# Kernel tuning notes

Measured on AMD Instinct MI355X. Metric: run time of the kernel, lower is better.

Reference implementation:

```python
import jax, jax.numpy as jnp
import numpy as np

N_NODES = 100000
N_EDGES = 3200000
D = 32


def _gat(x, edge_index, W, att_s, att_d, bias, heads, ch, neg_slope):
    """PyG-style GATConv (shared lin for src/dst, add_self_loops=False).
    x: [N, D_in], edge_index: [2, E], W: [heads*ch, D_in],
    att_s/att_d: [heads, ch], bias: [heads*ch]. Returns [N, heads*ch]."""
    n = x.shape[0]
    h = (x @ W.T).reshape(n, heads, ch)                      # [N,H,C]
    a_s = (h * att_s[None]).sum(-1)                           # [N,H]
    a_d = (h * att_d[None]).sum(-1)                           # [N,H]
    src, dst = edge_index[0], edge_index[1]
    logits = jax.nn.leaky_relu(a_s[src] + a_d[dst], neg_slope)  # [E,H]
    # segment softmax over edges grouped by destination node
    m = jax.ops.segment_max(logits, dst, num_segments=n)     # [N,H]
    m = jnp.where(jnp.isfinite(m), m, 0.0)                    # nodes w/ no in-edges
    ex = jnp.exp(logits - m[dst])                             # [E,H]
    denom = jax.ops.segment_sum(ex, dst, num_segments=n)     # [N,H]
    alpha = ex / (denom[dst] + 1e-16)                         # [E,H]
    out = jax.ops.segment_sum(alpha[:, :, None] * h[src], dst, num_segments=n)  # [N,H,C]
    return out.reshape(n, heads * ch) + bias


def setup_inputs() -> dict:
    key = jax.random.key(0)
    ks = jax.random.split(key, 16)
    x = jax.random.normal(ks[0], (N_NODES, D), dtype=jnp.float32)
    edge_index = jax.random.randint(ks[1], (2, N_EDGES), 0, N_NODES, dtype=jnp.int64)
    s = 1.0 / np.sqrt(D)
    return {
        "x": x,
        "edge_index": edge_index,
        "W1": jax.random.normal(ks[2], (32, D), dtype=jnp.float32) * s,
        "att_s1": jax.random.normal(ks[3], (2, 16), dtype=jnp.float32) * 0.05,
        "att_d1": jax.random.normal(ks[4], (2, 16), dtype=jnp.float32) * 0.05,
        "b1": jnp.full((32,), 0.1, dtype=jnp.float32),
        "ea1": jnp.ones((1,), dtype=jnp.float32),  # edge_activator
        "W2": jax.random.normal(ks[5], (32, 32), dtype=jnp.float32) * s,
        "att_s2": jax.random.normal(ks[6], (2, 16), dtype=jnp.float32) * 0.05,
        "att_d2": jax.random.normal(ks[7], (2, 16), dtype=jnp.float32) * 0.05,
        "b2": jnp.full((32,), 0.1, dtype=jnp.float32),
        "W3": jax.random.normal(ks[8], (32, 32), dtype=jnp.float32) * s,
        "att_s3": jax.random.normal(ks[9], (1, 32), dtype=jnp.float32) * 0.05,
        "att_d3": jax.random.normal(ks[10], (1, 32), dtype=jnp.float32) * 0.05,
        "b3": jnp.full((32,), 0.1, dtype=jnp.float32),
    }


def reference(x, edge_index, W1, att_s1, att_d1, b1, ea1,
              W2, att_s2, att_d2, b2, W3, att_s3, att_d3, b3):
    # --- layer 1 (negative_slope=0.01) ---
    h = _gat(x, edge_index, W1, att_s1, att_d1, b1, heads=2, ch=16, neg_slope=0.01)
    scale = jnp.tanh(ea1)[0]
    scale = jnp.where(scale < 0.1, 1.0, scale)  # 'continue' branch skips the scaling
    h = h * scale
    h = h + 0.05 * jax.lax.stop_gradient(h)      # h + 0.05*h.detach()
    h = jax.nn.elu(h)                            # eval path (training=False)
    h = jnp.clip(h, -3.0, 3.0)
    # --- layer 2 (default negative_slope=0.2) ---
    h = _gat(h, edge_index, W2, att_s2, att_d2, b2, heads=2, ch=16, neg_slope=0.2)
    h = jax.nn.elu(h)
    h = jnp.clip(h, -3.0, 3.0)
    # --- layer 3: heads=1, concat=False ---
    out = _gat(h, edge_index, W3, att_s3, att_d3, b3, heads=1, ch=32, neg_slope=0.2)
    return out
```

## Files before the change

### kernel.cpp

```cpp
#include <hip/hip_runtime.h>
#include <hip/hip_bf16.h>
#include <hip/hip_fp16.h>


#define NPB  128
#define CAPB 6144
#define PAD_SENTINEL 0xFFFFFFFFu

template <int H, int NL>
__device__ __forceinline__ void transform_body(
    const float* __restrict__ in, const float* __restrict__ W,
    const float* __restrict__ att_s, const float* __restrict__ att_d,
    __half* __restrict__ h16, float* __restrict__ a_s, float* __restrict__ a_d,
    int node0, int nlim, float (*Wl)[33], float (*xs)[32]) {
    constexpr int C = 32 / H;
    constexpr int NTH = NL * 32;
    int t = threadIdx.x;
    for (int i = t; i < 1024; i += NTH) Wl[i >> 5][i & 31] = W[i];
    int nl = t >> 5, o = t & 31;
    int node = node0 + nl;
    xs[nl][o] = (node < nlim) ? in[(size_t)node * 32 + o] : 0.f;
    __syncthreads();
    float acc = 0.f;
#pragma unroll
    for (int k = 0; k < 32; k++) acc = fmaf(xs[nl][k], Wl[o][k], acc);
    if (node < nlim) {
        h16[(size_t)node * 32 + o] = __float2half_rn(acc);
        float vs = acc * att_s[o];
        float vd = acc * att_d[o];
#pragma unroll
        for (int m = C / 2; m >= 1; m >>= 1) {
            vs += __shfl_xor(vs, m, 64);
            vd += __shfl_xor(vd, m, 64);
        }
        if ((o % C) == 0) {
            int hh = o / C;
            a_s[node * H + hh] = vs;
            a_d[node * H + hh] = vd;
        }
    }
}

__global__ void __launch_bounds__(1024)
k_bin_t1(const int* __restrict__ src, const int* __restrict__ dst,
         int* __restrict__ bucket_cursor, unsigned int* __restrict__ pairs,
         int e, int nb, int nbb,
         const float* __restrict__ in, const float* __restrict__ W,
         const float* __restrict__ att_s, const float* __restrict__ att_d,
         __half* __restrict__ h16, float* __restrict__ a_s,
         float* __restrict__ a_d, int nsplit) {
    __shared__ union {
        struct { int h[1024]; int bs[1024]; int cb[1024]; unsigned int stage[8192]; } b;
        struct { float Wl[32][33]; float xs[32][32]; } t;
    } sh;
    int t = threadIdx.x;
    if ((int)blockIdx.x >= nbb) {
        int node0 = ((int)blockIdx.x - nbb) * 32;
        transform_body<2, 32>(in, W, att_s, att_d, h16, a_s, a_d,
                              node0, nsplit, sh.t.Wl, sh.t.xs);
        return;
    }
    sh.b.h[t] = 0;
    __syncthreads();
    int e4 = e >> 2;
    int base4 = blockIdx.x * 2048;
    int boff[8];
    unsigned int pk[8];
#pragma unroll
    for (int k = 0; k < 2; k++) {
        int i4 = base4 + k * 1024 + t;
        if (i4 < e4) {
            int4 dv = ((const int4*)dst)[i4];
            int4 sv = ((const int4*)src)[i4];
            const int* dd = (const int*)&dv;
            const int* ss = (const int*)&sv;
#pragma unroll
            for (int j = 0; j < 4; j++) {
                int q = 4 * k + j;
                int d = dd[j];
                int b = d >> 7;
                pk[q] = ((unsigned int)ss[j] << 7) | (unsigned int)(d & 127);
                int off = atomicAdd(&sh.b.h[b], 1);
                boff[q] = (b << 16) | off;
            }
        } else {
#pragma unroll
            for (int j = 0; j < 4; j++) boff[4 * k + j] = -1;
        }
    }
    __syncthreads();
    if (t >= 128 && t - 128 < nb) {
        int b = t - 128;
        int c = sh.b.h[b];
        sh.b.cb[b] = c ? atomicAdd(&bucket_cursor[b], c) : 0;
    }
    if (t < 64) {
        int sum = 0;
#pragma unroll
        for (int j = 0; j < 16; j++) sum += sh.b.h[t * 16 + j];
        int run = sum;
#pragma unroll
        for (int off = 1; off < 64; off <<= 1) {
            int v = __shfl_up(run, off, 64);
            if (t >= off) run += v;
        }
        int base = run - sum;
#pragma unroll
        for (int j = 0; j < 16; j++) {
            int b = t * 16 + j;
            sh.b.bs[b] = base;
            base += sh.b.h[b];
        }
    }
    __syncthreads();
#pragma unroll
    for (int q = 0; q < 8; q++) {
        if (boff[q] >= 0) {
            int b = boff[q] >> 16;
            sh.b.stage[sh.b.bs[b] + (boff[q] & 0xFFFF)] = pk[q];
        }
    }
    __syncthreads();
    int wv = t >> 6, ln = t & 63;
    for (int b = wv; b < nb; b += 16) {
        int c = sh.b.h[b];
        if (c == 0) continue;
        int gb = sh.b.cb[b];
        int room = CAPB - gb;
        if (c > room) c = (room > 0) ? room : 0;
        unsigned int* dp = pairs + (size_t)b * CAPB + gb;
        const unsigned int* sp = sh.b.stage + sh.b.bs[b];
        for (int o = ln; o < c; o += 64) dp[o] = sp[o];
    }
    if (blockIdx.x == 0 && t < (e & 3)) {
        int i = (e & ~3) + t;
        int d = dst[i];
        int b = d >> 7;
        int r = atomicAdd(&bucket_cursor[b], 1);
        if (r < CAPB)
            pairs[(size_t)b * CAPB + r] =
                ((unsigned int)src[i] << 7) | (unsigned int)(d & 127);
    }
}

__global__ void __launch_bounds__(512)
k_sort_t1(const unsigned int* __restrict__ pairs,
          const int* __restrict__ bucket_cursor,
          int2* __restrict__ rowinfo, int* __restrict__ src_sorted,
          int n, int nb,
          const float* __restrict__ in, const float* __restrict__ W,
          const float* __restrict__ att_s, const float* __restrict__ att_d,
          __half* __restrict__ h16, float* __restrict__ a_s,
          float* __restrict__ a_d, int nsplit) {
    __shared__ union {
        struct { int cnt[NPB]; int cur[NPB]; int total;
                 unsigned int lp[CAPB]; int op[CAPB]; } s;
        struct { float Wl[32][33]; float xs[16][32]; } t;
    } sh;
    int t = threadIdx.x;
    if ((int)blockIdx.x >= nb) {
        int node0 = nsplit + ((int)blockIdx.x - nb) * 16;
        transform_body<2, 16>(in, W, att_s, att_d, h16, a_s, a_d,
                              node0, n, sh.t.Wl, sh.t.xs);
        return;
    }
    int b = blockIdx.x;
    int bbase = b * CAPB;
    int m = bucket_cursor[b];
    if (m > CAPB) m = CAPB;
    if (t < NPB) sh.s.cnt[t] = 0;
    __syncthreads();
    for (int cb = 0; cb < m; cb += 4096) {
        unsigned int pv[8];
#pragma unroll
        for (int u = 0; u < 8; u++) {
            int i = cb + u * 512 + t;
            pv[u] = (i < m) ? pairs[bbase + i] : PAD_SENTINEL;
        }
#pragma unroll
        for (int u = 0; u < 8; u++) {
            int i = cb + u * 512 + t;
            if (i < m) sh.s.lp[i] = pv[u];
            if (pv[u] != PAD_SENTINEL) atomicAdd(&sh.s.cnt[pv[u] & 127], 1);
        }
    }
    __syncthreads();
    if (t < 64) {
        int c0 = sh.s.cnt[2 * t];
        int c1 = sh.s.cnt[2 * t + 1];
        int sum = c0 + c1;
        int run = sum;
#pragma unroll
        for (int off = 1; off < 64; off <<= 1) {
            int v = __shfl_up(run, off, 64);
            if (t >= off) run += v;
        }
        int ex = run - sum;
        sh.s.cur[2 * t] = ex;
        sh.s.cur[2 * t + 1] = ex + c0;
        int node = b * NPB + 2 * t;
        if (node < n) rowinfo[node] = make_int2(bbase + ex, c0);
        if (node + 1 < n) rowinfo[node + 1] = make_int2(bbase + ex + c0, c1);
        if (t == 63) sh.s.total = run;
    }
    __syncthreads();
    for (int cb = 0; cb < m; cb += 4096) {
        unsigned int pv[8];
        int of[8];
#pragma unroll
        for (int u = 0; u < 8; u++) {
            int i = cb + u * 512 + t;
            pv[u] = (i < m) ? sh.s.lp[i] : PAD_SENTINEL;
        }
#pragma unroll
        for (int u = 0; u < 8; u++)
            if (pv[u] != PAD_SENTINEL) of[u] = atomicAdd(&sh.s.cur[pv[u] & 127], 1);
#pragma unroll
        for (int u = 0; u < 8; u++)
            if (pv[u] != PAD_SENTINEL) sh.s.op[of[u]] = (int)(pv[u] >> 7);
    }
    __syncthreads();
    int nt4 = (sh.s.total + 3) >> 2;
    int4* dst4 = (int4*)(src_sorted + bbase);
    const int4* src4 = (const int4*)sh.s.op;
    for (int i = t; i < nt4; i += 512) dst4[i] = src4[i];
}

#define PB_LOAD(Qa, Qb, Qc, Qd, H0, H1, H2_, H3_, H4_, H5_, H6_, H7_, B)      \
    Qa = *(const int4*)(lb + (B) * 2);                                        \
    Qb = *(const int4*)(lb + (B) * 2 + 8);                                    \
    Qc = *(const int4*)(lb + (B) * 2 + 16);                                   \
    Qd = *(const int4*)(lb + (B) * 2 + 24);                                   \
    H0 = *(const __half2*)(hbase + (unsigned)((Qa.x << 6) + co));             \
    H1 = *(const __half2*)(hbase + (unsigned)((Qa.z << 6) + co));             \
    H2_ = *(const __half2*)(hbase + (unsigned)((Qb.x << 6) + co));            \
    H3_ = *(const __half2*)(hbase + (unsigned)((Qb.z << 6) + co));            \
    H4_ = *(const __half2*)(hbase + (unsigned)((Qc.x << 6) + co));            \
    H5_ = *(const __half2*)(hbase + (unsigned)((Qc.z << 6) + co));            \
    H6_ = *(const __half2*)(hbase + (unsigned)((Qd.x << 6) + co));            \
    H7_ = *(const __half2*)(hbase + (unsigned)((Qd.z << 6) + co));

#define PB_FMA(Qa, Qb, Qc, Qd, H0, H1, H2_, H3_, H4_, H5_, H6_, H7_)          \
    {                                                                         \
        float xa0 = __int_as_float(Qa.y), xa1 = __int_as_float(Qa.w);         \
        float xb0 = __int_as_float(Qb.y), xb1 = __int_as_float(Qb.w);         \
        float xc0 = __int_as_float(Qc.y), xc1 = __int_as_float(Qc.w);         \
        float xd0 = __int_as_float(Qd.y), xd1 = __int_as_float(Qd.w);         \
        acc0 = fmaf(xa0, __half2float(__low2half(H0)), acc0);                 \
        acc1 = fmaf(xa0, __half2float(__high2half(H0)), acc1);                \
        acc0 = fmaf(xa1, __half2float(__low2half(H1)), acc0);                 \
        acc1 = fmaf(xa1, __half2float(__high2half(H1)), acc1);                \
        acc0 = fmaf(xb0, __half2float(__low2half(H2_)), acc0);                \
        acc1 = fmaf(xb0, __half2float(__high2half(H2_)), acc1);               \
        acc0 = fmaf(xb1, __half2float(__low2half(H3_)), acc0);                \
        acc1 = fmaf(xb1, __half2float(__high2half(H3_)), acc1);               \
        acc0 = fmaf(xc0, __half2float(__low2half(H4_)), acc0);                \
        acc1 = fmaf(xc0, __half2float(__high2half(H4_)), acc1);               \
        acc0 = fmaf(xc1, __half2float(__low2half(H5_)), acc0);                \
        acc1 = fmaf(xc1, __half2float(__high2half(H5_)), acc1);               \
        acc0 = fmaf(xd0, __half2float(__low2half(H6_)), acc0);                \
        acc1 = fmaf(xd0, __half2float(__high2half(H6_)), acc1);               \
        acc0 = fmaf(xd1, __half2float(__low2half(H7_)), acc0);                \
        acc1 = fmaf(xd1, __half2float(__high2half(H7_)), acc1);               \
    }

#define PB_PIPELINED_LOOP                                                     \
    {                                                                         \
        int4 qa, qb, qc, qd, na, nb2, nc, nd;                                 \
        __half2 h0, h1, h2, h3, h4, h5, h6, h7;                               \
        __half2 g0, g1, g2, g3, g4, g5, g6, g7;                               \
        PB_LOAD(qa, qb, qc, qd, h0, h1, h2, h3, h4, h5, h6, h7, 0)            \
        for (int base = 0; base < padB; base += 16) {                         \
            int nxt = base + 16;                                              \
            if (nxt < padB) {                                                 \
                PB_LOAD(na, nb2, nc, nd, g0, g1, g2, g3, g4, g5, g6, g7, nxt) \
            }                                                                 \
            PB_FMA(qa, qb, qc, qd, h0, h1, h2, h3, h4, h5, h6, h7)            \
            qa = na; qb = nb2; qc = nc; qd = nd;                              \
            h0 = g0; h1 = g1; h2 = g2; h3 = g3;                               \
            h4 = g4; h5 = g5; h6 = g6; h7 = g7;                               \
        }                                                                     \
    }

template <int H, int EPI, int H2>
__global__ void __launch_bounds__(256)
k_edge_f(const int2* __restrict__ rowinfo, const int* __restrict__ src_sorted,
         const __half* __restrict__ h16,
         const float* __restrict__ a_s, const float* __restrict__ a_d,
         const float* __restrict__ bias, const float* __restrict__ ea,
         const float* __restrict__ Wn, const float* __restrict__ att_sn,
         const float* __restrict__ att_dn,
         __half* __restrict__ h16n, float* __restrict__ a_sn,
         float* __restrict__ a_dn, int n, float slope) {
    constexpr int CAP = 96;
    constexpr int RSTR = 2 * CAP + 16;
    __shared__ int lds_raw[8][H][RSTR];
    __shared__ float Wl2[32][33];
    __shared__ float row[8][32];
    int t = threadIdx.x;
    for (int i = t; i < 1024; i += 256) Wl2[i >> 5][i & 31] = Wn[i];
    __syncthreads();
    int nw = t >> 5;
    int hl = t & 31;
    int node = blockIdx.x * 8 + nw;
    if (node >= n) return;
    float ats = att_sn[hl], atd = att_dn[hl];
    int2 bi = rowinfo[node];
    int beg = bi.x, deg = bi.y;
    int padB = (deg + 15) & ~15;

    float ad[H];
#pragma unroll
    for (int hh = 0; hh < H; hh++) ad[hh] = a_d[node * H + hh];

    float ds[H];
#pragma unroll
    for (int hh = 0; hh < H; hh++) ds[hh] = 0.f;
    bool fast = (padB <= CAP);
    if (fast) {
        for (int idx = hl; idx < padB; idx += 32) {
            if (idx < deg) {
                int s = src_sorted[beg + idx];
                if (H == 2) {
                    float2 as2 = *(const float2*)((const char*)a_s + (unsigned)(s << 3));
                    float l0 = as2.x + ad[0]; l0 = fmaxf(l0, l0 * slope);
                    float l1 = as2.y + ad[1]; l1 = fmaxf(l1, l1 * slope);
                    float e0 = __expf(l0), e1 = __expf(l1);
                    ds[0] += e0; ds[1] += e1;
                    ((int2*)lds_raw[nw][0])[idx] = make_int2(s, __float_as_int(e0));
                    ((int2*)lds_raw[nw][H - 1])[idx] = make_int2(s, __float_as_int(e1));
                } else {
                    float l0 = a_s[s] + ad[0]; l0 = fmaxf(l0, l0 * slope);
                    float e0 = __expf(l0);
                    ds[0] += e0;
                    ((int2*)lds_raw[nw][0])[idx] = make_int2(s, __float_as_int(e0));
                }
            } else {
#pragma unroll
                for (int hh = 0; hh < H; hh++)
                    ((int2*)lds_raw[nw][hh])[idx] = make_int2(0, 0);
            }
        }
    } else {
        for (int idx = hl; idx < deg; idx += 32) {
            int s = src_sorted[beg + idx];
            if (H == 2) {
                float2 as2 = *(const float2*)((const char*)a_s + (unsigned)(s << 3));
                float l0 = as2.x + ad[0]; l0 = fmaxf(l0, l0 * slope);
                float l1 = as2.y + ad[1]; l1 = fmaxf(l1, l1 * slope);
                ds[0] += __expf(l0); ds[1] += __expf(l1);
            } else {
                float l0 = a_s[s] + ad[0]; l0 = fmaxf(l0, l0 * slope);
                ds[0] += __expf(l0);
            }
        }
    }

    int e2 = hl >> 4;
    int l16 = hl & 15;
    int hd = (H == 2) ? (l16 >> 3) : 0;
    int co = l16 << 2;
    float adh = ad[hd];
    float acc0 = 0.f, acc1 = 0.f;
    const char* hbase = (const char*)h16;
    const int* lb = &lds_raw[nw][hd][e2 * 4];

    if (fast) {
        PB_PIPELINED_LOOP
    } else {
        for (int base = 0; base < deg; base += 16) {
#pragma unroll
            for (int u = 0; u < 8; u++) {
                int idx = base + u * 2 + e2;
                int s = 0;
                float ex = 0.f;
                if (idx < deg) {
                    s = src_sorted[beg + idx];
                    float l = a_s[s * H + hd] + adh;
                    l = fmaxf(l, l * slope);
                    ex = __expf(l);
                }
                __half2 hv = *(const __half2*)(hbase + (unsigned)((s << 6) + co));
                acc0 = fmaf(ex, __half2float(__low2half(hv)), acc0);
                acc1 = fmaf(ex, __half2float(__high2half(hv)), acc1);
            }
        }
    }

#pragma unroll
    for (int hh = 0; hh < H; hh++) {
        float v = ds[hh];
#pragma unroll
        for (int m = 16; m >= 1; m >>= 1) v += __shfl_xor(v, m, 64);
        ds[hh] = 1.f / (v + 1e-16f);
    }
    acc0 += __shfl_xor(acc0, 16, 64);
    acc1 += __shfl_xor(acc1, 16, 64);

    float invd = ds[hd];
    float2 bv = *(const float2*)(bias + l16 * 2);
    float v0 = fmaf(acc0, invd, bv.x);
    float v1 = fmaf(acc1, invd, bv.y);
    if (EPI == 1) {
        float s0 = tanhf(ea[0]);
        if (s0 < 0.1f) s0 = 1.0f;
        s0 *= 1.05f;
        v0 *= s0; v1 *= s0;
    }
    v0 = (v0 > 0.f) ? v0 : expm1f(v0);
    v1 = (v1 > 0.f) ? v1 : expm1f(v1);
    v0 = fminf(3.f, fmaxf(-3.f, v0));
    v1 = fminf(3.f, fmaxf(-3.f, v1));

    if (hl < 16) {
        row[nw][2 * l16] = v0;
        row[nw][2 * l16 + 1] = v1;
    }
    float acc = 0.f;
#pragma unroll
    for (int k = 0; k < 32; k++) acc = fmaf(row[nw][k], Wl2[hl][k], acc);
    h16n[(size_t)node * 32 + hl] = __float2half_rn(acc);
    float vs = acc * ats;
    float vd = acc * atd;
    constexpr int C2 = 32 / H2;
#pragma unroll
    for (int m = C2 / 2; m >= 1; m >>= 1) {
        vs += __shfl_xor(vs, m, 64);
        vd += __shfl_xor(vd, m, 64);
    }
    if ((hl % C2) == 0) {
        int hh = hl / C2;
        a_sn[node * H2 + hh] = vs;
        a_dn[node * H2 + hh] = vd;
    }
}

template <int H, int EPI>
__global__ void k_edge(const int2* __restrict__ rowinfo, const int* __restrict__ src_sorted,
                       const __half* __restrict__ h16,
                       const float* __restrict__ a_s, const float* __restrict__ a_d,
                       const float* __restrict__ bias, const float* __restrict__ ea,
                       float* __restrict__ out, int n, float slope) {
    constexpr int CAP = 96;
    constexpr int RSTR = 2 * CAP + 16;
    __shared__ int lds_raw[8][H][RSTR];
    int nw = threadIdx.x >> 5;
    int hl = threadIdx.x & 31;
    int node = blockIdx.x * 8 + nw;
    if (node >= n) return;
    int2 bi = rowinfo[node];
    int beg = bi.x, deg = bi.y;
    int padB = (deg + 15) & ~15;

    float ad[H];
#pragma unroll
    for (int hh = 0; hh < H; hh++) ad[hh] = a_d[node * H + hh];

    float ds[H];
#pragma unroll
    for (int hh = 0; hh < H; hh++) ds[hh] = 0.f;
    bool fast = (padB <= CAP);
    if (fast) {
        for (int idx = hl; idx < padB; idx += 32) {
            if (idx < deg) {
                int s = src_sorted[beg + idx];
                if (H == 2) {
                    float2 as2 = *(const float2*)((const char*)a_s + (unsigned)(s << 3));
                    float l0 = as2.x + ad[0]; l0 = fmaxf(l0, l0 * slope);
                    float l1 = as2.y + ad[1]; l1 = fmaxf(l1, l1 * slope);
                    float e0 = __expf(l0), e1 = __expf(l1);
                    ds[0] += e0; ds[1] += e1;
                    ((int2*)lds_raw[nw][0])[idx] = make_int2(s, __float_as_int(e0));
                    ((int2*)lds_raw[nw][H - 1])[idx] = make_int2(s, __float_as_int(e1));
                } else {
                    float l0 = a_s[s] + ad[0]; l0 = fmaxf(l0, l0 * slope);
                    float e0 = __expf(l0);
                    ds[0] += e0;
                    ((int2*)lds_raw[nw][0])[idx] = make_int2(s, __float_as_int(e0));
                }
            } else {
#pragma unroll
                for (int hh = 0; hh < H; hh++)
                    ((int2*)lds_raw[nw][hh])[idx] = make_int2(0, 0);
            }
        }
    } else {
        for (int idx = hl; idx < deg; idx += 32) {
            int s = src_sorted[beg + idx];
            if (H == 2) {
                float2 as2 = *(const float2*)((const char*)a_s + (unsigned)(s << 3));
                float l0 = as2.x + ad[0]; l0 = fmaxf(l0, l0 * slope);
                float l1 = as2.y + ad[1]; l1 = fmaxf(l1, l1 * slope);
                ds[0] += __expf(l0); ds[1] += __expf(l1);
            } else {
                float l0 = a_s[s] + ad[0]; l0 = fmaxf(l0, l0 * slope);
                ds[0] += __expf(l0);
            }
        }
    }

    int e2 = hl >> 4;
    int l16 = hl & 15;
    int hd = (H == 2) ? (l16 >> 3) : 0;
    int co = l16 << 2;
    float adh = ad[hd];
    float acc0 = 0.f, acc1 = 0.f;
    const char* hbase = (const char*)h16;
    const int* lb = &lds_raw[nw][hd][e2 * 4];

    if (fast) {
        PB_PIPELINED_LOOP
    } else {
        for (int base = 0; base < deg; base += 16) {
#pragma unroll
            for (int u = 0; u < 8; u++) {
                int idx = base + u * 2 + e2;
                int s = 0;
                float ex = 0.f;
                if (idx < deg) {
                    s = src_sorted[beg + idx];
                    float l = a_s[s * H + hd] + adh;
                    l = fmaxf(l, l * slope);
                    ex = __expf(l);
                }
                __half2 hv = *(const __half2*)(hbase + (unsigned)((s << 6) + co));
                acc0 = fmaf(ex, __half2float(__low2half(hv)), acc0);
                acc1 = fmaf(ex, __half2float(__high2half(hv)), acc1);
            }
        }
    }

#pragma unroll
    for (int hh = 0; hh < H; hh++) {
        float v = ds[hh];
#pragma unroll
        for (int m = 16; m >= 1; m >>= 1) v += __shfl_xor(v, m, 64);
        ds[hh] = 1.f / (v + 1e-16f);
    }
    acc0 += __shfl_xor(acc0, 16, 64);
    acc1 += __shfl_xor(acc1, 16, 64);

    if (l16 == hl) {
        float invd = ds[hd];
        float2 bv = *(const float2*)(bias + l16 * 2);
        float v0 = fmaf(acc0, invd, bv.x);
        float v1 = fmaf(acc1, invd, bv.y);
        if (EPI == 1) {
            float s0 = tanhf(ea[0]);
            if (s0 < 0.1f) s0 = 1.0f;
            s0 *= 1.05f;
            v0 *= s0; v1 *= s0;
            v0 = (v0 > 0.f) ? v0 : expm1f(v0);
            v1 = (v1 > 0.f) ? v1 : expm1f(v1);
            v0 = fminf(3.f, fmaxf(-3.f, v0));
            v1 = fminf(3.f, fmaxf(-3.f, v1));
        } else if (EPI == 2) {
            v0 = (v0 > 0.f) ? v0 : expm1f(v0);
            v1 = (v1 > 0.f) ? v1 : expm1f(v1);
            v0 = fminf(3.f, fmaxf(-3.f, v0));
            v1 = fminf(3.f, fmaxf(-3.f, v1));
        }
        *(float2*)(out + (size_t)node * 32 + l16 * 2) = make_float2(v0, v1);
    }
}

extern "C" void kernel_launch(void* const* d_in, const int* in_sizes, int n_in,
                              void* d_out, int out_size, void* d_ws, size_t ws_size,
                              hipStream_t stream) {
    const float* x   = (const float*)d_in[0];
    const int*   ei  = (const int*)d_in[1];
    const float* W1  = (const float*)d_in[2];
    const float* as1 = (const float*)d_in[3];
    const float* ad1 = (const float*)d_in[4];
    const float* b1  = (const float*)d_in[5];
    const float* ea1 = (const float*)d_in[6];
    const float* W2  = (const float*)d_in[7];
    const float* as2 = (const float*)d_in[8];
    const float* ad2 = (const float*)d_in[9];
    const float* b2  = (const float*)d_in[10];
    const float* W3  = (const float*)d_in[11];
    const float* as3 = (const float*)d_in[12];
    const float* ad3 = (const float*)d_in[13];
    const float* b3  = (const float*)d_in[14];
    float* out = (float*)d_out;

    const int n = in_sizes[0] / 32;
    const int e = in_sizes[1] / 2;
    const int* src = ei;
    const int* dst = ei + e;
    const int nb = (n + NPB - 1) / NPB;

    char* w = (char*)d_ws;
    auto alloc = [&](size_t bytes) -> void* {
        void* p = (void*)w;
        w += (bytes + 255) & ~(size_t)255;
        return p;
    };
    __half* h16a    = (__half*)alloc((size_t)n * 32 * 2);
    float* a_s1     = (float*)alloc((size_t)n * 2 * 4);
    float* a_d1     = (float*)alloc((size_t)n * 2 * 4);
    int2* rowinfo   = (int2*)alloc((size_t)n * 8);
    int* bucket_cur = (int*)alloc((size_t)(nb + 1) * 4);
    int* src_sorted = (int*)alloc((size_t)nb * CAPB * 4);
    unsigned int* pairs = (unsigned int*)alloc((size_t)nb * CAPB * 4);

    char* sc = (char*)pairs;
    auto carve = [&](size_t bytes) -> void* {
        void* p = (void*)sc;
        sc += (bytes + 255) & ~(size_t)255;
        return p;
    };
    __half* h16b = (__half*)carve((size_t)n * 32 * 2);
    float* a_s2  = (float*)carve((size_t)n * 2 * 4);
    float* a_d2  = (float*)carve((size_t)n * 2 * 4);
    float* a_s3  = (float*)carve((size_t)n * 4);
    float* a_d3  = (float*)carve((size_t)n * 4);

    int nsplit = n / 2;
    nsplit = (nsplit + 31) & ~31;
    if (nsplit > n) nsplit = n;
    const int t1a = (nsplit + 31) / 32;
    const int t1b = (n - nsplit + 15) / 16;
    int e4 = e >> 2;
    const int nbb = (e4 + 2047) / 2048;

    hipMemsetAsync(bucket_cur, 0, (size_t)nb * 4, stream);
    k_bin_t1<<<nbb + t1a, 1024, 0, stream>>>(src, dst, bucket_cur, pairs, e, nb, nbb,
                                             x, W1, as1, ad1, h16a, a_s1, a_d1, nsplit);
    k_sort_t1<<<nb + t1b, 512, 0, stream>>>(pairs, bucket_cur, rowinfo, src_sorted, n, nb,
                                            x, W1, as1, ad1, h16a, a_s1, a_d1, nsplit);

    const int egrid = (n + 7) / 8;

    k_edge_f<2, 1, 2><<<egrid, 256, 0, stream>>>(rowinfo, src_sorted, h16a, a_s1, a_d1,
                                                 b1, ea1, W2, as2, ad2,
                                                 h16b, a_s2, a_d2, n, 0.01f);
    k_edge_f<2, 2, 1><<<egrid, 256, 0, stream>>>(rowinfo, src_sorted, h16b, a_s2, a_d2,
                                                 b2, nullptr, W3, as3, ad3,
                                                 h16a, a_s3, a_d3, n, 0.2f);
    k_edge<1, 0><<<egrid, 256, 0, stream>>>(rowinfo, src_sorted, h16a, a_s3, a_d3,
                                            b3, nullptr, out, n, 0.2f);
}
```

Before: 307.5 us.

## Gather full 16-byte feature chunks per lane with 8 edges per pass

Changes the edge aggregation lane mapping in both edge kernels. Each group of 4 lanes now covers one edge and each lane loads an int4 (8 halves) of the source row, so 8 edges are processed per pass instead of each lane loading a 4-byte half2 across 16-edge pipelined blocks. The intent is fewer, wider gather instructions per edge. In exchange it drops the explicit software prefetch pipeline, adds a 3-step 8-register shuffle reduction, and runs the epilogue with 8 values per lane using float4 stores.

```diff
diff --git a/kernel.cpp b/kernel.cpp
--- a/kernel.cpp
+++ b/kernel.cpp
@@ -226,60 +226,20 @@
     for (int i = t; i < nt4; i += 512) dst4[i] = src4[i];
 }
 
-#define PB_LOAD(Qa, Qb, Qc, Qd, H0, H1, H2_, H3_, H4_, H5_, H6_, H7_, B)      \
-    Qa = *(const int4*)(lb + (B) * 2);                                        \
-    Qb = *(const int4*)(lb + (B) * 2 + 8);                                    \
-    Qc = *(const int4*)(lb + (B) * 2 + 16);                                   \
-    Qd = *(const int4*)(lb + (B) * 2 + 24);                                   \
-    H0 = *(const __half2*)(hbase + (unsigned)((Qa.x << 6) + co));             \
-    H1 = *(const __half2*)(hbase + (unsigned)((Qa.z << 6) + co));             \
-    H2_ = *(const __half2*)(hbase + (unsigned)((Qb.x << 6) + co));            \
-    H3_ = *(const __half2*)(hbase + (unsigned)((Qb.z << 6) + co));            \
-    H4_ = *(const __half2*)(hbase + (unsigned)((Qc.x << 6) + co));            \
-    H5_ = *(const __half2*)(hbase + (unsigned)((Qc.z << 6) + co));            \
-    H6_ = *(const __half2*)(hbase + (unsigned)((Qd.x << 6) + co));            \
-    H7_ = *(const __half2*)(hbase + (unsigned)((Qd.z << 6) + co));
-
-#define PB_FMA(Qa, Qb, Qc, Qd, H0, H1, H2_, H3_, H4_, H5_, H6_, H7_)          \
+#define PB25_FMA(HV)                                                          \
     {                                                                         \
-        float xa0 = __int_as_float(Qa.y), xa1 = __int_as_float(Qa.w);         \
-        float xb0 = __int_as_float(Qb.y), xb1 = __int_as_float(Qb.w);         \
-        float xc0 = __int_as_float(Qc.y), xc1 = __int_as_float(Qc.w);         \
-        float xd0 = __int_as_float(Qd.y), xd1 = __int_as_float(Qd.w);         \
-        acc0 = fmaf(xa0, __half2float(__low2half(H0)), acc0);                 \
-        acc1 = fmaf(xa0, __half2float(__high2half(H0)), acc1);                \
-        acc0 = fmaf(xa1, __half2float(__low2half(H1)), acc0);                 \
-        acc1 = fmaf(xa1, __half2float(__high2half(H1)), acc1);                \
-        acc0 = fmaf(xb0, __half2float(__low2half(H2_)), acc0);                \
-        acc1 = fmaf(xb0, __half2float(__high2half(H2_)), acc1);               \
-        acc0 = fmaf(xb1, __half2float(__low2half(H3_)), acc0);                \
-        acc1 = fmaf(xb1, __half2float(__high2half(H3_)), acc1);               \
-        acc0 = fmaf(xc0, __half2float(__low2half(H4_)), acc0);                \
-        acc1 = fmaf(xc0, __half2float(__high2half(H4_)), acc1);               \
-        acc0 = fmaf(xc1, __half2float(__low2half(H5_)), acc0);                \
-        acc1 = fmaf(xc1, __half2float(__high2half(H5_)), acc1);               \
-        acc0 = fmaf(xd0, __half2float(__low2half(H6_)), acc0);                \
-        acc1 = fmaf(xd0, __half2float(__high2half(H6_)), acc1);               \
-        acc0 = fmaf(xd1, __half2float(__low2half(H7_)), acc0);                \
-        acc1 = fmaf(xd1, __half2float(__high2half(H7_)), acc1);               \
-    }
-
-#define PB_PIPELINED_LOOP                                                     \
-    {                                                                         \
-        int4 qa, qb, qc, qd, na, nb2, nc, nd;                                 \
-        __half2 h0, h1, h2, h3, h4, h5, h6, h7;                               \
-        __half2 g0, g1, g2, g3, g4, g5, g6, g7;                               \
-        PB_LOAD(qa, qb, qc, qd, h0, h1, h2, h3, h4, h5, h6, h7, 0)            \
-        for (int base = 0; base < padB; base += 16) {                         \
-            int nxt = base + 16;                                              \
-            if (nxt < padB) {                                                 \
-                PB_LOAD(na, nb2, nc, nd, g0, g1, g2, g3, g4, g5, g6, g7, nxt) \
-            }                                                                 \
-            PB_FMA(qa, qb, qc, qd, h0, h1, h2, h3, h4, h5, h6, h7)            \
-            qa = na; qb = nb2; qc = nc; qd = nd;                              \
-            h0 = g0; h1 = g1; h2 = g2; h3 = g3;                               \
-            h4 = g4; h5 = g5; h6 = g6; h7 = g7;                               \
-        }                                                                     \
+        __half2 p0 = *(__half2*)&HV.x;                                        \
+        __half2 p1 = *(__half2*)&HV.y;                                        \
+        __half2 p2 = *(__half2*)&HV.z;                                        \
+        __half2 p3 = *(__half2*)&HV.w;                                        \
+        av[0] = fmaf(ex, __half2float(__low2half(p0)), av[0]);                \
+        av[1] = fmaf(ex, __half2float(__high2half(p0)), av[1]);               \
+        av[2] = fmaf(ex, __half2float(__low2half(p1)), av[2]);                \
+        av[3] = fmaf(ex, __half2float(__high2half(p1)), av[3]);               \
+        av[4] = fmaf(ex, __half2float(__low2half(p2)), av[4]);                \
+        av[5] = fmaf(ex, __half2float(__high2half(p2)), av[5]);               \
+        av[6] = fmaf(ex, __half2float(__low2half(p3)), av[6]);                \
+        av[7] = fmaf(ex, __half2float(__high2half(p3)), av[7]);               \
     }
 
 template <int H, int EPI, int H2>
@@ -356,35 +316,43 @@
         }
     }
 
-    int e2 = hl >> 4;
-    int l16 = hl & 15;
-    int hd = (H == 2) ? (l16 >> 3) : 0;
-    int co = l16 << 2;
-    float adh = ad[hd];
-    float acc0 = 0.f, acc1 = 0.f;
+    int q4 = hl & 3;
+    int eo = hl >> 2;
+    int hd2 = (H == 2) ? (q4 >> 1) : 0;
+    float adh = ad[hd2];
+    float av[8];
+#pragma unroll
+    for (int k = 0; k < 8; k++) av[k] = 0.f;
     const char* hbase = (const char*)h16;
-    const int* lb = &lds_raw[nw][hd][e2 * 4];
+    const int2* stp = (const int2*)&lds_raw[nw][hd2][0];
 
     if (fast) {
-        PB_PIPELINED_LOOP
+        for (int base = 0; base < padB; base += 8) {
+            int2 se = stp[base + eo];
+            float ex = __int_as_float(se.y);
+            int4 hv = *(const int4*)(hbase + (unsigned)((se.x << 6) + (q4 << 4)));
+            PB25_FMA(hv)
+        }
     } else {
-        for (int base = 0; base < deg; base += 16) {
-#pragma unroll
-            for (int u = 0; u < 8; u++) {
-                int idx = base + u * 2 + e2;
-                int s = 0;
-                float ex = 0.f;
-                if (idx < deg) {
-                    s = src_sorted[beg + idx];
-                    float l = a_s[s * H + hd] + adh;
-                    l = fmaxf(l, l * slope);
-                    ex = __expf(l);
-                }
-                __half2 hv = *(const __half2*)(hbase + (unsigned)((s << 6) + co));
-                acc0 = fmaf(ex, __half2float(__low2half(hv)), acc0);
-                acc1 = fmaf(ex, __half2float(__high2half(hv)), acc1);
-            }
-        }
+        for (int base = 0; base < deg; base += 8) {
+            int idx = base + eo;
+            int s = 0;
+            float ex = 0.f;
+            if (idx < deg) {
+                s = src_sorted[beg + idx];
+                float l = a_s[s * H + hd2] + adh;
+                l = fmaxf(l, l * slope);
+                ex = __expf(l);
+            }
+            int4 hv = *(const int4*)(hbase + (unsigned)((s << 6) + (q4 << 4)));
+            PB25_FMA(hv)
+        }
+    }
+
+#pragma unroll
+    for (int m = 4; m <= 16; m <<= 1) {
+#pragma unroll
+        for (int k = 0; k < 8; k++) av[k] += __shfl_xor(av[k], m, 64);
     }
 
 #pragma unroll
@@ -394,28 +362,37 @@
         for (int m = 16; m >= 1; m >>= 1) v += __shfl_xor(v, m, 64);
         ds[hh] = 1.f / (v + 1e-16f);
     }
-    acc0 += __shfl_xor(acc0, 16, 64);
-    acc1 += __shfl_xor(acc1, 16, 64);
-
-    float invd = ds[hd];
-    float2 bv = *(const float2*)(bias + l16 * 2);
-    float v0 = fmaf(acc0, invd, bv.x);
-    float v1 = fmaf(acc1, invd, bv.y);
+    float invd = ds[hd2];
+
+    float4 bv0 = *(const float4*)(bias + q4 * 8);
+    float4 bv1 = *(const float4*)(bias + q4 * 8 + 4);
+    float v[8];
+    v[0] = fmaf(av[0], invd, bv0.x);
+    v[1] = fmaf(av[1], invd, bv0.y);
+    v[2] = fmaf(av[2], invd, bv0.z);
+    v[3] = fmaf(av[3], invd, bv0.w);
+    v[4] = fmaf(av[4], invd, bv1.x);
+    v[5] = fmaf(av[5], invd, bv1.y);
+    v[6] = fmaf(av[6], invd, bv1.z);
+    v[7] = fmaf(av[7], invd, bv1.w);
     if (EPI == 1) {
         float s0 = tanhf(ea[0]);
         if (s0 < 0.1f) s0 = 1.0f;
         s0 *= 1.05f;
-        v0 *= s0; v1 *= s0;
-    }
-    v0 = (v0 > 0.f) ? v0 : expm1f(v0);
-    v1 = (v1 > 0.f) ? v1 : expm1f(v1);
-    v0 = fminf(3.f, fmaxf(-3.f, v0));
-    v1 = fminf(3.f, fmaxf(-3.f, v1));
-
-    if (hl < 16) {
-        row[nw][2 * l16] = v0;
-        row[nw][2 * l16 + 1] = v1;
-    }
+#pragma unroll
+        for (int k = 0; k < 8; k++) v[k] *= s0;
+    }
+#pragma unroll
+    for (int k = 0; k < 8; k++) {
+        v[k] = (v[k] > 0.f) ? v[k] : expm1f(v[k]);
+        v[k] = fminf(3.f, fmaxf(-3.f, v[k]));
+    }
+
+    if (eo == 0) {
+        *(float4*)&row[nw][q4 * 8]     = make_float4(v[0], v[1], v[2], v[3]);
+        *(float4*)&row[nw][q4 * 8 + 4] = make_float4(v[4], v[5], v[6], v[7]);
+    }
+
     float acc = 0.f;
 #pragma unroll
     for (int k = 0; k < 32; k++) acc = fmaf(row[nw][k], Wl2[hl][k], acc);
@@ -499,35 +476,43 @@
         }
     }
 
-    int e2 = hl >> 4;
-    int l16 = hl & 15;
-    int hd = (H == 2) ? (l16 >> 3) : 0;
-    int co = l16 << 2;
-    float adh = ad[hd];
-    float acc0 = 0.f, acc1 = 0.f;
+    int q4 = hl & 3;
+    int eo = hl >> 2;
+    int hd2 = (H == 2) ? (q4 >> 1) : 0;
+    float adh = ad[hd2];
+    float av[8];
+#pragma unroll
+    for (int k = 0; k < 8; k++) av[k] = 0.f;
     const char* hbase = (const char*)h16;
-    const int* lb = &lds_raw[nw][hd][e2 * 4];
+    const int2* stp = (const int2*)&lds_raw[nw][hd2][0];
 
     if (fast) {
-        PB_PIPELINED_LOOP
+        for (int base = 0; base < padB; base += 8) {
+            int2 se = stp[base + eo];
+            float ex = __int_as_float(se.y);
+            int4 hv = *(const int4*)(hbase + (unsigned)((se.x << 6) + (q4 << 4)));
+            PB25_FMA(hv)
+        }
     } else {
-        for (int base = 0; base < deg; base += 16) {
-#pragma unroll
-            for (int u = 0; u < 8; u++) {
-                int idx = base + u * 2 + e2;
-                int s = 0;
-                float ex = 0.f;
-                if (idx < deg) {
-                    s = src_sorted[beg + idx];
-                    float l = a_s[s * H + hd] + adh;
-                    l = fmaxf(l, l * slope);
-                    ex = __expf(l);
-                }
-                __half2 hv = *(const __half2*)(hbase + (unsigned)((s << 6) + co));
-                acc0 = fmaf(ex, __half2float(__low2half(hv)), acc0);
-                acc1 = fmaf(ex, __half2float(__high2half(hv)), acc1);
-            }
-        }
+        for (int base = 0; base < deg; base += 8) {
+            int idx = base + eo;
+            int s = 0;
+            float ex = 0.f;
+            if (idx < deg) {
+                s = src_sorted[beg + idx];
+                float l = a_s[s * H + hd2] + adh;
+                l = fmaxf(l, l * slope);
+                ex = __expf(l);
+            }
+            int4 hv = *(const int4*)(hbase + (unsigned)((s << 6) + (q4 << 4)));
+            PB25_FMA(hv)
+        }
+    }
+
+#pragma unroll
+    for (int m = 4; m <= 16; m <<= 1) {
+#pragma unroll
+        for (int k = 0; k < 8; k++) av[k] += __shfl_xor(av[k], m, 64);
     }
 
 #pragma unroll
@@ -537,30 +522,37 @@
         for (int m = 16; m >= 1; m >>= 1) v += __shfl_xor(v, m, 64);
         ds[hh] = 1.f / (v + 1e-16f);
     }
-    acc0 += __shfl_xor(acc0, 16, 64);
-    acc1 += __shfl_xor(acc1, 16, 64);
-
-    if (l16 == hl) {
-        float invd = ds[hd];
-        float2 bv = *(const float2*)(bias + l16 * 2);
-        float v0 = fmaf(acc0, invd, bv.x);
-        float v1 = fmaf(acc1, invd, bv.y);
+    float invd = ds[hd2];
+
+    if (eo == 0) {
+        float4 bv0 = *(const float4*)(bias + q4 * 8);
+        float4 bv1 = *(const float4*)(bias + q4 * 8 + 4);
+        float v[8];
+        v[0] = fmaf(av[0], invd, bv0.x);
+        v[1] = fmaf(av[1], invd, bv0.y);
+        v[2] = fmaf(av[2], invd, bv0.z);
+        v[3] = fmaf(av[3], invd, bv0.w);
+        v[4] = fmaf(av[4], invd, bv1.x);
+        v[5] = fmaf(av[5], invd, bv1.y);
+        v[6] = fmaf(av[6], invd, bv1.z);
+        v[7] = fmaf(av[7], invd, bv1.w);
         if (EPI == 1) {
             float s0 = tanhf(ea[0]);
             if (s0 < 0.1f) s0 = 1.0f;
             s0 *= 1.05f;
-            v0 *= s0; v1 *= s0;
-            v0 = (v0 > 0.f) ? v0 : expm1f(v0);
-            v1 = (v1 > 0.f) ? v1 : expm1f(v1);
-            v0 = fminf(3.f, fmaxf(-3.f, v0));
-            v1 = fminf(3.f, fmaxf(-3.f, v1));
-        } else if (EPI == 2) {
-            v0 = (v0 > 0.f) ? v0 : expm1f(v0);
-            v1 = (v1 > 0.f) ? v1 : expm1f(v1);
-            v0 = fminf(3.f, fmaxf(-3.f, v0));
-            v1 = fminf(3.f, fmaxf(-3.f, v1));
-        }
-        *(float2*)(out + (size_t)node * 32 + l16 * 2) = make_float2(v0, v1);
+#pragma unroll
+            for (int k = 0; k < 8; k++) v[k] *= s0;
+        }
+        if (EPI == 1 || EPI == 2) {
+#pragma unroll
+            for (int k = 0; k < 8; k++) {
+                v[k] = (v[k] > 0.f) ? v[k] : expm1f(v[k]);
+                v[k] = fminf(3.f, fmaxf(-3.f, v[k]));
+            }
+        }
+        float* op = out + (size_t)node * 32 + q4 * 8;
+        *(float4*)op       = make_float4(v[0], v[1], v[2], v[3]);
+        *(float4*)(op + 4) = make_float4(v[4], v[5], v[6], v[7]);
     }
 }
 
```

Result: slower. 330.0 us (+7.3%).
